# Optimization experiments

Hardware: AMD Instinct MI355X
Metric: run time of the kernel (lower is better)

Reference implementation:

```python
import jax, jax.numpy as jnp
import numpy as np

N, D, H1, H2, C, K = 8192, 512, 1024, 512, 10, 64
EPS_BN = 1e-5  # torch BatchNorm1d default eps


def _bn(x, g, b):
    # BatchNorm1d in training mode: per-batch stats, biased variance
    mu = x.mean(axis=0)
    var = x.var(axis=0)
    return (x - mu) / jnp.sqrt(var + EPS_BN) * g + b


def _features(x, ibn_g, ibn_b, W1, b1, g1, bb1, W2, b2, g2, bb2):
    x = _bn(x, ibn_g, ibn_b)                    # input_norm
    h = _bn(jnp.tanh(x @ W1.T + b1), g1, bb1)   # layer 1: Linear -> Tanh -> BN
    h = _bn(jnp.tanh(h @ W2.T + b2), g2, bb2)   # layer 2
    return h                                    # [N, H2]


def _nona_self(fx, fn, y_ohe):
    # sim = -cdist(fx, fn); self-neighbor path (x == x_n): -inf diag + top-k mask
    sq_x = jnp.sum(fx * fx, axis=1)
    sq_n = jnp.sum(fn * fn, axis=1)
    d2 = jnp.maximum(sq_x[:, None] + sq_n[None, :] - 2.0 * (fx @ fn.T), 0.0)
    safe = d2 > 1e-9
    dist = jnp.where(safe, jnp.sqrt(jnp.where(safe, d2, 1.0)), 0.0)
    sim = -dist
    eye = jnp.eye(N, dtype=bool)
    sim = jnp.where(eye, -jnp.inf, sim)         # sim -= inf * I
    _, idx = jax.lax.top_k(sim, K)              # [N, K]
    keep = jnp.zeros((N, N), dtype=bool).at[jnp.arange(N)[:, None], idx].set(True)
    sim = jnp.where(keep, sim, -jnp.inf)        # KNNMask: non-topk -> -inf
    probs = jax.nn.softmax(sim, axis=1)
    return jnp.clip(probs @ y_ohe, 0.0, 1.0)


def setup_inputs() -> dict:
    key = jax.random.key(0)
    ks = jax.random.split(key, 6)
    x = jax.random.normal(ks[0], (N, D), dtype=jnp.float32)
    x_n = x + 0.0  # NONA self-neighbor mode requires x_n == x elementwise
    y_n = jax.random.randint(ks[1], (N,), 0, C, dtype=jnp.int32)
    s1 = 1.0 / np.sqrt(D)
    s2 = 1.0 / np.sqrt(H1)
    W1 = jax.random.uniform(ks[2], (H1, D), jnp.float32, -s1, s1)
    b1 = jax.random.uniform(ks[3], (H1,), jnp.float32, -s1, s1)
    W2 = jax.random.uniform(ks[4], (H2, H1), jnp.float32, -s2, s2)
    b2 = jax.random.uniform(ks[5], (H2,), jnp.float32, -s2, s2)
    return {
        "x": x, "x_n": x_n, "y_n": y_n,
        "ibn_g": jnp.ones((D,), jnp.float32), "ibn_b": jnp.zeros((D,), jnp.float32),
        "W1": W1, "b1": b1, "g1": jnp.ones((H1,), jnp.float32), "bb1": jnp.zeros((H1,), jnp.float32),
        "W2": W2, "b2": b2, "g2": jnp.ones((H2,), jnp.float32), "bb2": jnp.zeros((H2,), jnp.float32),
    }


def reference(x, x_n, y_n, ibn_g, ibn_b, W1, b1, g1, bb1, W2, b2, g2, bb2):
    fx = _features(x, ibn_g, ibn_b, W1, b1, g1, bb1, W2, b2, g2, bb2)
    fn = _features(x_n, ibn_g, ibn_b, W1, b1, g1, bb1, W2, b2, g2, bb2)
    y_ohe = jax.nn.one_hot(y_n, C, dtype=jnp.float32)
    return _nona_self(fx, fn, y_ohe)
```

## Files before the change

kernel.cpp:

```cpp
#include <hip/hip_runtime.h>
#include <math.h>

#define NROWS 8192
#define DIM   512
#define HID1  1024
#define HID2  512
#define NCLS  10
#define KTOP  64
#define KPACK 1024
#define KFULL 1536
#define EPSBAND 0.02f

typedef __attribute__((ext_vector_type(8))) short short8;
typedef __attribute__((ext_vector_type(4))) float f32x4;
typedef __attribute__((ext_vector_type(4))) double f64x4;

__device__ __forceinline__ unsigned short f2bf(float x) {
    unsigned u = __float_as_uint(x);
    u += 0x7FFFu + ((u >> 16) & 1u);
    return (unsigned short)(u >> 16);
}
__device__ __forceinline__ float bf2f(unsigned short h) {
    return __uint_as_float(((unsigned)h) << 16);
}

template <typename T>
__global__ __launch_bounds__(256) void col_stats_partial(
    const T* __restrict__ A, int F, int rowsPerBlock,
    double* __restrict__ pSum, double* __restrict__ pSqs)
{
    int c  = blockIdx.x * 256 + threadIdx.x;
    int r0 = blockIdx.y * rowsPerBlock;
    double s = 0.0, s2 = 0.0;
    for (int r = r0; r < r0 + rowsPerBlock; ++r) {
        double v = (double)A[(size_t)r * F + c];
        s  += v;
        s2 += v * v;
    }
    pSum[(size_t)blockIdx.y * F + c] = s;
    pSqs[(size_t)blockIdx.y * F + c] = s2;
}

__global__ __launch_bounds__(256) void col_stats_final(
    const double* __restrict__ pSum, const double* __restrict__ pSqs,
    const float* __restrict__ g, const float* __restrict__ b,
    double* __restrict__ scale, double* __restrict__ shift, int F, int nPart)
{
    int c = blockIdx.x * 256 + threadIdx.x;
    double s = 0.0, s2 = 0.0;
    for (int p = 0; p < nPart; ++p) {
        s  += pSum[(size_t)p * F + c];
        s2 += pSqs[(size_t)p * F + c];
    }
    double mean = s * (1.0 / NROWS);
    double var  = s2 * (1.0 / NROWS) - mean * mean;
    double sc   = (double)g[c] / sqrt(var + 1e-5);
    scale[c] = sc;
    shift[c] = (double)b[c] - mean * sc;
}

template <typename T>
__global__ __launch_bounds__(256) void gemm_mfma_tanh(
    const T* __restrict__ A, const double* __restrict__ scl, const double* __restrict__ sft,
    const float* __restrict__ W, const float* __restrict__ bias,
    double* __restrict__ out, int Kd, int F)
{
    __shared__ double aS[32 * 66];
    __shared__ double bS[32 * 66];
    const int t = threadIdx.x;
    const int lane = t & 63;
    const int wv = t >> 6;
    const int fBase = blockIdx.x * 64;
    const int mBase = blockIdx.y * 64;
    const int srow = t >> 2;
    const int skq  = (t & 3) * 8;

    f64x4 acc[4];
    #pragma unroll
    for (int n = 0; n < 4; ++n) acc[n] = (f64x4){0.0, 0.0, 0.0, 0.0};

    const int nChunks = Kd >> 5;
    for (int ch = 0; ch < nChunks; ++ch) {
        const int kb = ch << 5;
        double av[8];
        if constexpr (sizeof(T) == 4) {
            const float4* ap = (const float4*)&A[(size_t)(mBase + srow) * Kd + kb + skq];
            float4 a0 = ap[0], a1 = ap[1];
            av[0] = a0.x; av[1] = a0.y; av[2] = a0.z; av[3] = a0.w;
            av[4] = a1.x; av[5] = a1.y; av[6] = a1.z; av[7] = a1.w;
        } else {
            const double2* ap = (const double2*)&A[(size_t)(mBase + srow) * Kd + kb + skq];
            double2 d0 = ap[0], d1 = ap[1], d2 = ap[2], d3 = ap[3];
            av[0] = d0.x; av[1] = d0.y; av[2] = d1.x; av[3] = d1.y;
            av[4] = d2.x; av[5] = d2.y; av[6] = d3.x; av[7] = d3.y;
        }
        #pragma unroll
        for (int i = 0; i < 8; ++i)
            av[i] = av[i] * scl[kb + skq + i] + sft[kb + skq + i];
        #pragma unroll
        for (int i = 0; i < 8; ++i)
            aS[(skq + i) * 66 + srow] = av[i];
        const float4* wp = (const float4*)&W[(size_t)(fBase + srow) * Kd + kb + skq];
        float4 w0 = wp[0], w1 = wp[1];
        bS[(skq + 0) * 66 + srow] = (double)w0.x;
        bS[(skq + 1) * 66 + srow] = (double)w0.y;
        bS[(skq + 2) * 66 + srow] = (double)w0.z;
        bS[(skq + 3) * 66 + srow] = (double)w0.w;
        bS[(skq + 4) * 66 + srow] = (double)w1.x;
        bS[(skq + 5) * 66 + srow] = (double)w1.y;
        bS[(skq + 6) * 66 + srow] = (double)w1.z;
        bS[(skq + 7) * 66 + srow] = (double)w1.w;
        __syncthreads();
        #pragma unroll
        for (int k4 = 0; k4 < 8; ++k4) {
            const int kk = k4 * 4 + (lane >> 4);
            double a = aS[kk * 66 + wv * 16 + (lane & 15)];
            #pragma unroll
            for (int n = 0; n < 4; ++n) {
                double b = bS[kk * 66 + n * 16 + (lane & 15)];
                acc[n] = __builtin_amdgcn_mfma_f64_16x16x4f64(a, b, acc[n], 0, 0, 0);
            }
        }
        __syncthreads();
    }

    #pragma unroll
    for (int n = 0; n < 4; ++n) {
        const int f = fBase + n * 16 + (lane & 15);
        const double bz = (double)bias[f];
        #pragma unroll
        for (int r = 0; r < 4; ++r) {
            const int m = mBase + wv * 16 + (lane >> 4) * 4 + r;
            out[(size_t)m * F + f] = tanh(acc[n][r] + bz);
        }
    }
}

__global__ __launch_bounds__(256) void pack_features(
    const double* __restrict__ y2, const double* __restrict__ scl, const double* __restrict__ sft,
    unsigned short* __restrict__ R, float* __restrict__ sqf)
{
    __shared__ double red[4];
    const int r = blockIdx.x;
    const int t = threadIdx.x;
    const int wid = t >> 6, lane = t & 63;
    const int c = t * 2;
    double2 y  = *(const double2*)&y2[(size_t)r * HID2 + c];
    double2 s2 = *(const double2*)&scl[c];
    double2 h2 = *(const double2*)&sft[c];
    double f0 = y.x * s2.x + h2.x;
    double f1 = y.y * s2.y + h2.y;
    unsigned short hi0 = f2bf((float)f0);
    unsigned short hi1 = f2bf((float)f1);
    unsigned short lo0 = f2bf((float)(f0 - (double)bf2f(hi0)));
    unsigned short lo1 = f2bf((float)(f1 - (double)bf2f(hi1)));
    unsigned short* Rr = R + (size_t)r * KPACK;
    Rr[c]           = hi0; Rr[c + 1]           = hi1;
    Rr[HID2 + c]    = lo0; Rr[HID2 + c + 1]    = lo1;
    double s = f0 * f0 + f1 * f1;
    #pragma unroll
    for (int off = 32; off > 0; off >>= 1) s += __shfl_down(s, off);
    if (lane == 0) red[wid] = s;
    __syncthreads();
    if (t == 0) sqf[r] = (float)(red[0] + red[1] + red[2] + red[3]);
}

__global__ __launch_bounds__(256) void sim_mfma(
    const unsigned short* __restrict__ R, const float* __restrict__ sqf,
    float* __restrict__ simbuf, int rowBase)
{
    __shared__ unsigned short aT[128 * 64];
    __shared__ unsigned short bT[128 * 64];
    const int t = threadIdx.x;
    const int wid = t >> 6, lane = t & 63;
    const int wr = wid >> 1, wc = wid & 1;
    const int iBase = rowBase + blockIdx.y * 128;
    const int jBase = blockIdx.x * 128;
    const int srow = lane >> 3;
    const int skk  = (lane & 7) * 8;

    f32x4 zero = {0.f, 0.f, 0.f, 0.f};
    f32x4 acc[4][4];
    #pragma unroll
    for (int m = 0; m < 4; ++m)
        #pragma unroll
        for (int n = 0; n < 4; ++n) acc[m][n] = zero;

    for (int k0 = 0; k0 < KFULL; k0 += 64) {
        const int aSrc = (k0 < 512)  ? k0 : (k0 - 512);
        const int bSrc = (k0 < 1024) ? k0 : (k0 - 1024);
        #pragma unroll
        for (int c = 0; c < 4; ++c) {
            int row = c * 32 + wid * 8 + srow;
            const unsigned short* gpA = R + (size_t)(iBase + row) * KPACK + aSrc + skk;
            const unsigned short* gpB = R + (size_t)(jBase + row) * KPACK + bSrc + skk;
            unsigned short* lpA = &aT[(c * 4 + wid) * 512];
            unsigned short* lpB = &bT[(c * 4 + wid) * 512];
            __builtin_amdgcn_global_load_lds((const __attribute__((address_space(1))) void*)gpA,
                (__attribute__((address_space(3))) void*)lpA, 16, 0, 0);
            __builtin_amdgcn_global_load_lds((const __attribute__((address_space(1))) void*)gpB,
                (__attribute__((address_space(3))) void*)lpB, 16, 0, 0);
        }
        __syncthreads();
        #pragma unroll
        for (int ks = 0; ks < 2; ++ks) {
            short8 aF[4], bF[4];
            #pragma unroll
            for (int m = 0; m < 4; ++m) {
                int rA = wr * 64 + m * 16 + (lane & 15);
                aF[m] = *(const short8*)&aT[rA * 64 + ks * 32 + (lane >> 4) * 8];
            }
            #pragma unroll
            for (int n = 0; n < 4; ++n) {
                int rB = wc * 64 + n * 16 + (lane & 15);
                bF[n] = *(const short8*)&bT[rB * 64 + ks * 32 + (lane >> 4) * 8];
            }
            #pragma unroll
            for (int m = 0; m < 4; ++m)
                #pragma unroll
                for (int n = 0; n < 4; ++n)
                    acc[m][n] = __builtin_amdgcn_mfma_f32_16x16x32_bf16(aF[m], bF[n], acc[m][n], 0, 0, 0);
        }
        __syncthreads();
    }

    #pragma unroll
    for (int m = 0; m < 4; ++m) {
        #pragma unroll
        for (int n = 0; n < 4; ++n) {
            int j = jBase + wc * 64 + n * 16 + (lane & 15);
            float sqj = sqf[j];
            #pragma unroll
            for (int r = 0; r < 4; ++r) {
                int i = iBase + wr * 64 + m * 16 + (lane >> 4) * 4 + r;
                float d2 = sqf[i] + sqj - 2.0f * acc[m][n][r];
                d2 = fmaxf(d2, 0.f);
                float s = (i == j) ? -INFINITY : -d2;
                simbuf[(size_t)(i - rowBase) * NROWS + j] = s;
            }
        }
    }
}

__device__ __forceinline__ unsigned fKey(float v) {
    unsigned b = __float_as_uint(v);
    return (b & 0x80000000u) ? ~b : (b | 0x80000000u);
}
__device__ __forceinline__ float keyToFloat(unsigned k) {
    unsigned b = (k & 0x80000000u) ? (k ^ 0x80000000u) : ~k;
    return __uint_as_float(b);
}

__global__ __launch_bounds__(256) void topk_refine(
    const float* __restrict__ simbuf,
    const double* __restrict__ y2, const double* __restrict__ scl, const double* __restrict__ sft,
    const int* __restrict__ labels, float* __restrict__ out, int rowBase)
{
    __shared__ int      redI[4];
    __shared__ unsigned redU[4];
    __shared__ float    redF[4];
    __shared__ float    cls[NCLS];
    __shared__ int      bandJ[128];
    __shared__ double   bandD2[128];
    __shared__ unsigned char keepB[128];
    __shared__ int      bandCnt;

    const int t = threadIdx.x;
    const int wid = t >> 6, lane = t & 63;
    const int row = blockIdx.x;
    const int gi = rowBase + row;
    const float* srow = simbuf + (size_t)row * NROWS;

    unsigned key[32];
    #pragma unroll
    for (int ii = 0; ii < 32; ++ii) key[ii] = fKey(srow[t + ii * 256]);

    unsigned kmax = 0u;
    #pragma unroll
    for (int ii = 0; ii < 32; ++ii) kmax = max(kmax, key[ii]);
    #pragma unroll
    for (int off = 32; off > 0; off >>= 1) kmax = max(kmax, (unsigned)__shfl_down(kmax, off));
    if (lane == 0) redU[wid] = kmax;
    if (t == 0) bandCnt = 0;
    if (t < NCLS) cls[t] = 0.f;
    __syncthreads();
    kmax = max(max(redU[0], redU[1]), max(redU[2], redU[3]));
    float d2min = fmaxf(-keyToFloat(kmax), 0.f);
    float distMin = (d2min > 1e-9f) ? sqrtf(d2min) : 0.f;
    __syncthreads();

    unsigned lo = 0u, hi = 0xFFFFFFFFu;
    while (lo < hi) {
        unsigned mid = (unsigned)(((unsigned long long)lo + hi + 1ull) >> 1);
        int cnt = 0;
        #pragma unroll
        for (int ii = 0; ii < 32; ++ii) cnt += (key[ii] >= mid) ? 1 : 0;
        #pragma unroll
        for (int off = 32; off > 0; off >>= 1) cnt += __shfl_down(cnt, off);
        if (lane == 0) redI[wid] = cnt;
        __syncthreads();
        int tot = redI[0] + redI[1] + redI[2] + redI[3];
        __syncthreads();
        if (tot >= KTOP) lo = mid; else hi = mid - 1u;
    }
    const float s64 = keyToFloat(lo);
    const unsigned Ku = fKey(s64 + EPSBAND);
    const unsigned Kl = fKey(s64 - EPSBAND);

    int cnt = 0;
    #pragma unroll
    for (int ii = 0; ii < 32; ++ii) cnt += (key[ii] >= Ku) ? 1 : 0;
    #pragma unroll
    for (int off = 32; off > 0; off >>= 1) cnt += __shfl_down(cnt, off);
    if (lane == 0) redI[wid] = cnt;
    __syncthreads();
    const int nSafe = redI[0] + redI[1] + redI[2] + redI[3];
    const int Rslots = KTOP - nSafe;

    #pragma unroll
    for (int ii = 0; ii < 32; ++ii) {
        if (key[ii] >= Kl && key[ii] < Ku) {
            int pos = atomicAdd(&bandCnt, 1);
            if (pos < 128) bandJ[pos] = t + ii * 256;
        }
    }
    __syncthreads();
    const int nb = min(bandCnt, 128);

    for (int c2 = wid; c2 < nb; c2 += 4) {
        int j = bandJ[c2];
        double s = 0.0;
        for (int d = lane; d < HID2; d += 64) {
            double sc = scl[d], sh = sft[d];
            double fi = y2[(size_t)gi * HID2 + d] * sc + sh;
            double fj = y2[(size_t)j  * HID2 + d] * sc + sh;
            double df = fi - fj;
            s += df * df;
        }
        #pragma unroll
        for (int off = 32; off > 0; off >>= 1) s += __shfl_down(s, off);
        if (lane == 0) bandD2[c2] = s;
    }
    __syncthreads();

    for (int c2 = t; c2 < nb; c2 += 256) {
        double d2c = bandD2[c2];
        int jc = bandJ[c2];
        int rank = 0;
        for (int q = 0; q < nb; ++q) {
            double dq = bandD2[q];
            rank += (dq < d2c || (dq == d2c && bandJ[q] < jc)) ? 1 : 0;
        }
        keepB[c2] = (rank < Rslots) ? 1 : 0;
    }
    __syncthreads();

    float S = 0.f;
    #pragma unroll
    for (int ii = 0; ii < 32; ++ii) {
        if (key[ii] >= Ku) {
            float d2 = -keyToFloat(key[ii]);
            float dist = (d2 > 1e-9f) ? sqrtf(d2) : 0.f;
            float w = expf(distMin - dist);
            S += w;
            atomicAdd(&cls[labels[t + ii * 256]], w);
        }
    }
    for (int c2 = t; c2 < nb; c2 += 256) {
        if (keepB[c2]) {
            double dd = bandD2[c2];
            float dist = (dd > 1e-9) ? (float)sqrt(dd) : 0.f;
            float w = expf(distMin - dist);
            S += w;
            atomicAdd(&cls[labels[bandJ[c2]]], w);
        }
    }
    #pragma unroll
    for (int off = 32; off > 0; off >>= 1) S += __shfl_down(S, off);
    if (lane == 0) redF[wid] = S;
    __syncthreads();
    float Stot = redF[0] + redF[1] + redF[2] + redF[3];

    if (t < NCLS) {
        float p = cls[t] / Stot;
        out[(size_t)gi * NCLS + t] = fminf(fmaxf(p, 0.f), 1.f);
    }
}

extern "C" void kernel_launch(void* const* d_in, const int* in_sizes, int n_in,
                              void* d_out, int out_size, void* d_ws, size_t ws_size,
                              hipStream_t stream)
{
    const float* x     = (const float*)d_in[0];
    const int*   y_n   = (const int*)d_in[2];
    const float* ibn_g = (const float*)d_in[3];
    const float* ibn_b = (const float*)d_in[4];
    const float* W1    = (const float*)d_in[5];
    const float* b1    = (const float*)d_in[6];
    const float* g1    = (const float*)d_in[7];
    const float* bb1   = (const float*)d_in[8];
    const float* W2    = (const float*)d_in[9];
    const float* b2    = (const float*)d_in[10];
    const float* g2    = (const float*)d_in[11];
    const float* bb2   = (const float*)d_in[12];
    float* out = (float*)d_out;

    char* ws = (char*)d_ws;
    double*         y1   = (double*)(ws);
    float*          simb = (float*)(ws);
    unsigned short* Rp   = (unsigned short*)(ws + 33554432);
    double*         y2   = (double*)(ws + 67108864);
    double*         pSum = (double*)(ws + 100663296);
    double*         pSqs = (double*)(ws + 101187584);
    double*         prm  = (double*)(ws + 101711872);
    double* scale0 = prm;           double* shift0 = prm + 1024;
    double* scale1 = prm + 2048;    double* shift1 = prm + 3072;
    double* scale2 = prm + 4096;    double* shift2 = prm + 5120;
    float*          sqf  = (float*)(ws + 101761024);

    dim3 blk(256);
    const int RPB = NROWS / 64;

    col_stats_partial<float><<<dim3(DIM / 256, 64), blk, 0, stream>>>(x, DIM, RPB, pSum, pSqs);
    col_stats_final<<<dim3(DIM / 256), blk, 0, stream>>>(pSum, pSqs, ibn_g, ibn_b, scale0, shift0, DIM, 64);
    gemm_mfma_tanh<float><<<dim3(HID1 / 64, NROWS / 64), blk, 0, stream>>>(x, scale0, shift0, W1, b1, y1, DIM, HID1);
    col_stats_partial<double><<<dim3(HID1 / 256, 64), blk, 0, stream>>>(y1, HID1, RPB, pSum, pSqs);
    col_stats_final<<<dim3(HID1 / 256), blk, 0, stream>>>(pSum, pSqs, g1, bb1, scale1, shift1, HID1, 64);
    gemm_mfma_tanh<double><<<dim3(HID2 / 64, NROWS / 64), blk, 0, stream>>>(y1, scale1, shift1, W2, b2, y2, HID1, HID2);
    col_stats_partial<double><<<dim3(HID2 / 256, 64), blk, 0, stream>>>(y2, HID2, RPB, pSum, pSqs);
    col_stats_final<<<dim3(HID2 / 256), blk, 0, stream>>>(pSum, pSqs, g2, bb2, scale2, shift2, HID2, 64);
    pack_features<<<dim3(NROWS), blk, 0, stream>>>(y2, scale2, shift2, Rp, sqf);
    for (int ch = 0; ch < 8; ++ch) {
        int rowBase = ch * 1024;
        sim_mfma<<<dim3(NROWS / 128, 1024 / 128), blk, 0, stream>>>(Rp, sqf, simb, rowBase);
        topk_refine<<<dim3(1024), blk, 0, stream>>>(simb, y2, scale2, shift2, y_n, out, rowBase);
    }
}
```

Baseline: 1.347 ms.

## Double-buffer LDS in both GEMMs and remap workgroups across XCDs

Both the f64 MFMA GEMM and the bf16 similarity GEMM now use two LDS buffers, so the next K-chunk is fetched from global memory while the current one is computed, and only one barrier is needed per iteration. The GEMM grids are flattened and workgroup ids are remapped in an XCD-aware (mod 8) order so that neighbouring tiles share L2. The f64 GEMM also changes its LDS padding stride from 66 to 67 and loads scale and shift as vectors. The cost is double the LDS footprint and more live registers, which may lower occupancy.

Measured after the change: 1.363 ms. No clear change (+1.2%).

```diff
diff --git a/kernel.cpp b/kernel.cpp
--- a/kernel.cpp
+++ b/kernel.cpp
@@ -65,13 +65,20 @@
     const float* __restrict__ W, const float* __restrict__ bias,
     double* __restrict__ out, int Kd, int F)
 {
-    __shared__ double aS[32 * 66];
-    __shared__ double bS[32 * 66];
+    __shared__ double aS[2][32 * 67];
+    __shared__ double bS[2][32 * 67];
     const int t = threadIdx.x;
     const int lane = t & 63;
     const int wv = t >> 6;
-    const int fBase = blockIdx.x * 64;
-    const int mBase = blockIdx.y * 64;
+    const int nwg = gridDim.x;
+    const int q = nwg >> 3;
+    const int bid = blockIdx.x;
+    const int wgid = (bid & 7) * q + (bid >> 3);
+    const int fBlocks = F >> 6;
+    const int mb = wgid / fBlocks;
+    const int fb = wgid - mb * fBlocks;
+    const int fBase = fb * 64;
+    const int mBase = mb * 64;
     const int srow = t >> 2;
     const int skq  = (t & 3) * 8;
 
@@ -79,49 +86,69 @@
     #pragma unroll
     for (int n = 0; n < 4; ++n) acc[n] = (f64x4){0.0, 0.0, 0.0, 0.0};
 
-    const int nChunks = Kd >> 5;
-    for (int ch = 0; ch < nChunks; ++ch) {
+    T      areg[8];
+    float  wreg[8];
+    double sclr[8], sftr[8];
+
+    auto stage_load = [&](int ch) {
         const int kb = ch << 5;
-        double av[8];
+        const T* ap = &A[(size_t)(mBase + srow) * Kd + kb + skq];
         if constexpr (sizeof(T) == 4) {
-            const float4* ap = (const float4*)&A[(size_t)(mBase + srow) * Kd + kb + skq];
-            float4 a0 = ap[0], a1 = ap[1];
-            av[0] = a0.x; av[1] = a0.y; av[2] = a0.z; av[3] = a0.w;
-            av[4] = a1.x; av[5] = a1.y; av[6] = a1.z; av[7] = a1.w;
+            float4 x0 = *(const float4*)ap;
+            float4 x1 = *(const float4*)(ap + 4);
+            areg[0] = x0.x; areg[1] = x0.y; areg[2] = x0.z; areg[3] = x0.w;
+            areg[4] = x1.x; areg[5] = x1.y; areg[6] = x1.z; areg[7] = x1.w;
         } else {
-            const double2* ap = (const double2*)&A[(size_t)(mBase + srow) * Kd + kb + skq];
-            double2 d0 = ap[0], d1 = ap[1], d2 = ap[2], d3 = ap[3];
-            av[0] = d0.x; av[1] = d0.y; av[2] = d1.x; av[3] = d1.y;
-            av[4] = d2.x; av[5] = d2.y; av[6] = d3.x; av[7] = d3.y;
-        }
-        #pragma unroll
-        for (int i = 0; i < 8; ++i)
-            av[i] = av[i] * scl[kb + skq + i] + sft[kb + skq + i];
-        #pragma unroll
-        for (int i = 0; i < 8; ++i)
-            aS[(skq + i) * 66 + srow] = av[i];
+            const double2* dp = (const double2*)ap;
+            double2 d0 = dp[0], d1 = dp[1], d2 = dp[2], d3 = dp[3];
+            areg[0] = d0.x; areg[1] = d0.y; areg[2] = d1.x; areg[3] = d1.y;
+            areg[4] = d2.x; areg[5] = d2.y; areg[6] = d3.x; areg[7] = d3.y;
+        }
         const float4* wp = (const float4*)&W[(size_t)(fBase + srow) * Kd + kb + skq];
         float4 w0 = wp[0], w1 = wp[1];
-        bS[(skq + 0) * 66 + srow] = (double)w0.x;
-        bS[(skq + 1) * 66 + srow] = (double)w0.y;
-        bS[(skq + 2) * 66 + srow] = (double)w0.z;
-        bS[(skq + 3) * 66 + srow] = (double)w0.w;
-        bS[(skq + 4) * 66 + srow] = (double)w1.x;
-        bS[(skq + 5) * 66 + srow] = (double)w1.y;
-        bS[(skq + 6) * 66 + srow] = (double)w1.z;
-        bS[(skq + 7) * 66 + srow] = (double)w1.w;
-        __syncthreads();
+        wreg[0] = w0.x; wreg[1] = w0.y; wreg[2] = w0.z; wreg[3] = w0.w;
+        wreg[4] = w1.x; wreg[5] = w1.y; wreg[6] = w1.z; wreg[7] = w1.w;
+        const double2* sp = (const double2*)&scl[kb + skq];
+        const double2* hp = (const double2*)&sft[kb + skq];
+        #pragma unroll
+        for (int i = 0; i < 4; ++i) {
+            double2 sv = sp[i], hv = hp[i];
+            sclr[2 * i] = sv.x; sclr[2 * i + 1] = sv.y;
+            sftr[2 * i] = hv.x; sftr[2 * i + 1] = hv.y;
+        }
+    };
+    auto stage_write = [&](int buf) {
+        #pragma unroll
+        for (int i = 0; i < 8; ++i) {
+            aS[buf][(skq + i) * 67 + srow] = (double)areg[i] * sclr[i] + sftr[i];
+            bS[buf][(skq + i) * 67 + srow] = (double)wreg[i];
+        }
+    };
+    auto compute = [&](int buf) {
         #pragma unroll
         for (int k4 = 0; k4 < 8; ++k4) {
             const int kk = k4 * 4 + (lane >> 4);
-            double a = aS[kk * 66 + wv * 16 + (lane & 15)];
+            double a = aS[buf][kk * 67 + wv * 16 + (lane & 15)];
             #pragma unroll
             for (int n = 0; n < 4; ++n) {
-                double b = bS[kk * 66 + n * 16 + (lane & 15)];
+                double b = bS[buf][kk * 67 + n * 16 + (lane & 15)];
                 acc[n] = __builtin_amdgcn_mfma_f64_16x16x4f64(a, b, acc[n], 0, 0, 0);
             }
         }
+    };
+
+    const int nChunks = Kd >> 5;
+    stage_load(0);
+    stage_write(0);
+    __syncthreads();
+    int cur = 0;
+    for (int ch = 0; ch < nChunks; ++ch) {
+        const bool hn = (ch + 1 < nChunks);
+        if (hn) stage_load(ch + 1);
+        compute(cur);
+        if (hn) stage_write(cur ^ 1);
         __syncthreads();
+        cur ^= 1;
     }
 
     #pragma unroll
@@ -169,13 +196,17 @@
     const unsigned short* __restrict__ R, const float* __restrict__ sqf,
     float* __restrict__ simbuf, int rowBase)
 {
-    __shared__ unsigned short aT[128 * 64];
-    __shared__ unsigned short bT[128 * 64];
+    __shared__ unsigned short aT[2][128 * 64];
+    __shared__ unsigned short bT[2][128 * 64];
     const int t = threadIdx.x;
     const int wid = t >> 6, lane = t & 63;
     const int wr = wid >> 1, wc = wid & 1;
-    const int iBase = rowBase + blockIdx.y * 128;
-    const int jBase = blockIdx.x * 128;
+    const int bid  = blockIdx.y * 8 + blockIdx.x;
+    const int wgid = (bid & 7) * 64 + (bid >> 3);
+    const int ib = wgid & 7;
+    const int jb = wgid >> 3;
+    const int iBase = rowBase + ib * 128;
+    const int jBase = jb * 128;
     const int srow = lane >> 3;
     const int skk  = (lane & 7) * 8;
 
@@ -186,34 +217,42 @@
         #pragma unroll
         for (int n = 0; n < 4; ++n) acc[m][n] = zero;
 
-    for (int k0 = 0; k0 < KFULL; k0 += 64) {
+    auto STAGE = [&](int buf, int kt) {
+        const int k0 = kt * 64;
         const int aSrc = (k0 < 512)  ? k0 : (k0 - 512);
         const int bSrc = (k0 < 1024) ? k0 : (k0 - 1024);
         #pragma unroll
         for (int c = 0; c < 4; ++c) {
-            int row = c * 32 + wid * 8 + srow;
+            const int row = c * 32 + wid * 8 + srow;
             const unsigned short* gpA = R + (size_t)(iBase + row) * KPACK + aSrc + skk;
             const unsigned short* gpB = R + (size_t)(jBase + row) * KPACK + bSrc + skk;
-            unsigned short* lpA = &aT[(c * 4 + wid) * 512];
-            unsigned short* lpB = &bT[(c * 4 + wid) * 512];
+            unsigned short* lpA = &aT[buf][(c * 4 + wid) * 512];
+            unsigned short* lpB = &bT[buf][(c * 4 + wid) * 512];
             __builtin_amdgcn_global_load_lds((const __attribute__((address_space(1))) void*)gpA,
                 (__attribute__((address_space(3))) void*)lpA, 16, 0, 0);
             __builtin_amdgcn_global_load_lds((const __attribute__((address_space(1))) void*)gpB,
                 (__attribute__((address_space(3))) void*)lpB, 16, 0, 0);
         }
-        __syncthreads();
+    };
+
+    STAGE(0, 0);
+    __syncthreads();
+    int cur = 0;
+    const int nKT = KFULL / 64;
+    for (int kt = 0; kt < nKT; ++kt) {
+        if (kt + 1 < nKT) STAGE(cur ^ 1, kt + 1);
         #pragma unroll
         for (int ks = 0; ks < 2; ++ks) {
             short8 aF[4], bF[4];
             #pragma unroll
             for (int m = 0; m < 4; ++m) {
                 int rA = wr * 64 + m * 16 + (lane & 15);
-                aF[m] = *(const short8*)&aT[rA * 64 + ks * 32 + (lane >> 4) * 8];
+                aF[m] = *(const short8*)&aT[cur][rA * 64 + ks * 32 + (lane >> 4) * 8];
             }
             #pragma unroll
             for (int n = 0; n < 4; ++n) {
                 int rB = wc * 64 + n * 16 + (lane & 15);
-                bF[n] = *(const short8*)&bT[rB * 64 + ks * 32 + (lane >> 4) * 8];
+                bF[n] = *(const short8*)&bT[cur][rB * 64 + ks * 32 + (lane >> 4) * 8];
             }
             #pragma unroll
             for (int m = 0; m < 4; ++m)
@@ -222,6 +261,7 @@
                     acc[m][n] = __builtin_amdgcn_mfma_f32_16x16x32_bf16(aF[m], bF[n], acc[m][n], 0, 0, 0);
         }
         __syncthreads();
+        cur ^= 1;
     }
 
     #pragma unroll
@@ -423,16 +463,16 @@
 
     col_stats_partial<float><<<dim3(DIM / 256, 64), blk, 0, stream>>>(x, DIM, RPB, pSum, pSqs);
     col_stats_final<<<dim3(DIM / 256), blk, 0, stream>>>(pSum, pSqs, ibn_g, ibn_b, scale0, shift0, DIM, 64);
-    gemm_mfma_tanh<float><<<dim3(HID1 / 64, NROWS / 64), blk, 0, stream>>>(x, scale0, shift0, W1, b1, y1, DIM, HID1);
+    gemm_mfma_tanh<float><<<dim3((NROWS / 64) * (HID1 / 64)), blk, 0, stream>>>(x, scale0, shift0, W1, b1, y1, DIM, HID1);
     col_stats_partial<double><<<dim3(HID1 / 256, 64), blk, 0, stream>>>(y1, HID1, RPB, pSum, pSqs);
     col_stats_final<<<dim3(HID1 / 256), blk, 0, stream>>>(pSum, pSqs, g1, bb1, scale1, shift1, HID1, 64);
-    gemm_mfma_tanh<double><<<dim3(HID2 / 64, NROWS / 64), blk, 0, stream>>>(y1, scale1, shift1, W2, b2, y2, HID1, HID2);
+    gemm_mfma_tanh<double><<<dim3((NROWS / 64) * (HID2 / 64)), blk, 0, stream>>>(y1, scale1, shift1, W2, b2, y2, HID1, HID2);
     col_stats_partial<double><<<dim3(HID2 / 256, 64), blk, 0, stream>>>(y2, HID2, RPB, pSum, pSqs);
     col_stats_final<<<dim3(HID2 / 256), blk, 0, stream>>>(pSum, pSqs, g2, bb2, scale2, shift2, HID2, 64);
     pack_features<<<dim3(NROWS), blk, 0, stream>>>(y2, scale2, shift2, Rp, sqf);
     for (int ch = 0; ch < 8; ++ch) {
         int rowBase = ch * 1024;
-        sim_mfma<<<dim3(NROWS / 128, 1024 / 128), blk, 0, stream>>>(Rp, sqf, simb, rowBase);
+        sim_mfma<<<dim3(8, 64), blk, 0, stream>>>(Rp, sqf, simb, rowBase);
         topk_refine<<<dim3(1024), blk, 0, stream>>>(simb, y2, scale2, shift2, y_n, out, rowBase);
     }
 }
```
